# Kernel tuning notes

Measured on AMD Instinct MI355X. Metric: run time of the kernel, lower is better.

Reference implementation:

```python
import jax, jax.numpy as jnp
import numpy as np

NUM_HEADS = 8  # matches init_kwargs num_heads
LN_EPS = 1e-5  # torch.nn.LayerNorm default


def setup_inputs() -> dict:
    key = jax.random.key(0)
    ks = jax.random.split(key, 12)
    E, B, H, S = 16384, 16, 256, 32
    edge_features = jax.random.normal(ks[0], (E, H), jnp.float32)
    edge_coords = jax.random.normal(ks[1], (E, 3), jnp.float32)
    # sorted, equal-size segments (all graphs non-empty)
    batch = jnp.repeat(jnp.arange(B, dtype=jnp.int32), E // B)
    s_h = 1.0 / np.sqrt(H)
    s_sh = 1.0 / np.sqrt(S * H)
    seed_vectors = jax.random.normal(ks[2], (S, H), jnp.float32)
    # weights stored [in, out] (transposed vs torch nn.Linear)
    Wq = jax.random.normal(ks[3], (H, H), jnp.float32) * s_h
    Wk = jax.random.normal(ks[4], (H, H), jnp.float32) * s_h
    Wv = jax.random.normal(ks[5], (H, H), jnp.float32) * s_h
    Wo = jax.random.normal(ks[6], (H, H), jnp.float32) * s_h
    bo = jnp.zeros((H,), jnp.float32)
    ln_g = jnp.ones((H,), jnp.float32)
    ln_b = jnp.zeros((H,), jnp.float32)
    W1 = jax.random.normal(ks[7], (S * H, H), jnp.float32) * s_sh
    b1 = jnp.zeros((H,), jnp.float32)
    W2 = jax.random.normal(ks[8], (H, H), jnp.float32) * s_h
    b2 = jnp.zeros((H,), jnp.float32)
    return dict(edge_features=edge_features, edge_coords=edge_coords, batch=batch,
                seed_vectors=seed_vectors, Wq=Wq, Wk=Wk, Wv=Wv, Wo=Wo, bo=bo,
                ln_g=ln_g, ln_b=ln_b, W1=W1, b1=b1, W2=W2, b2=b2, num_graphs=B)


def reference(edge_features, edge_coords, batch, seed_vectors, Wq, Wk, Wv, Wo, bo,
              ln_g, ln_b, W1, b1, W2, b2, num_graphs):
    S, H = seed_vectors.shape
    nh = NUM_HEADS
    hd = H // nh
    q = (seed_vectors @ Wq).reshape(S, nh, hd)          # shared across graphs
    k = (edge_features @ Wk).reshape(-1, nh, hd)        # [E, nh, hd]
    v = (edge_features @ Wv).reshape(-1, nh, hd)
    scores = jnp.einsum('shd,ehd->esh', q, k) / np.sqrt(hd).astype(np.float32)
    # segment softmax over edges within each graph
    m = jax.lax.stop_gradient(jax.ops.segment_max(scores, batch, num_segments=num_graphs))
    num = jnp.exp(scores - m[batch])
    den = jax.ops.segment_sum(num, batch, num_segments=num_graphs)
    w = num / den[batch]                                # [E, S, nh]
    att = jax.ops.segment_sum(jnp.einsum('esh,ehd->eshd', w, v), batch,
                              num_segments=num_graphs)  # [B, S, nh, hd]
    att = att.reshape(num_graphs, S, H)                 # concat heads (head-major)
    y = seed_vectors[None, :, :] + att @ Wo + bo        # residual + out_proj
    mu = jnp.mean(y, axis=-1, keepdims=True)
    var = jnp.mean((y - mu) ** 2, axis=-1, keepdims=True)
    y = (y - mu) / jnp.sqrt(var + LN_EPS) * ln_g + ln_b
    flat = y.reshape(num_graphs, S * H)
    h1 = jax.nn.silu(flat @ W1 + b1)
    return h1 @ W2 + b2                                 # [B, H]
```

## Files before the change

### kernel.cpp

```cpp
#include <hip/hip_runtime.h>
#include <math.h>
#include <stdint.h>

#define E_EDGES 16384
#define H_DIM   256
#define S_SEEDS 32
#define NHEADS  8
#define HDIM    32
#define BGRAPHS 16
#define EPG     1024
#define NCHUNK  256
#define CPG     16
#define RSQRT_HD 0.17677669529663687f

typedef __attribute__((ext_vector_type(8))) short bf16x8;
typedef __attribute__((ext_vector_type(4))) float f32x4;

__device__ inline unsigned short f2bf(float x) {
    unsigned u = __float_as_uint(x);
    u += 0x7fff + ((u >> 16) & 1);
    return (unsigned short)(u >> 16);
}
__device__ inline float bf2f(unsigned int h) {
    return __uint_as_float((h & 0xffffu) << 16);
}
__device__ inline unsigned pack2(float a, float b) {
    return (unsigned)f2bf(a) | ((unsigned)f2bf(b) << 16);
}

__global__ __launch_bounds__(256) void k_wc(const float* __restrict__ Wv,
                                            const float* __restrict__ Wk,
                                            const float* __restrict__ Wq,
                                            const float* __restrict__ seed,
                                            unsigned short* __restrict__ WcT) {
    int j = blockIdx.x;
    int i = threadIdx.x;
    float val;
    if (j < H_DIM) {
        val = Wv[i * H_DIM + j];
    } else {
        int c = j - H_DIM;
        int h = c >> 5, s = c & 31;
        __shared__ float qp[8][33];
        __shared__ float qrow[HDIM];
        int d = i & 31, g = i >> 5;
        const float* wq = &Wq[(g * 32) * H_DIM + h * HDIM + d];
        const float* sd = &seed[s * H_DIM + g * 32];
        float p = 0.f;
        #pragma unroll
        for (int ii = 0; ii < 32; ++ii)
            p = fmaf(sd[ii], wq[(size_t)ii * H_DIM], p);
        qp[g][d] = p;
        __syncthreads();
        if (i < HDIM) {
            float qv = 0.f;
            #pragma unroll
            for (int g2 = 0; g2 < 8; ++g2) qv += qp[g2][i];
            qrow[i] = qv;
        }
        __syncthreads();
        const float* wk = &Wk[i * H_DIM + h * HDIM];
        float acc = 0.f;
        #pragma unroll
        for (int dd = 0; dd < HDIM; dd += 4) {
            float4 w = *(const float4*)&wk[dd];
            float4 qq = *(const float4*)&qrow[dd];
            acc = fmaf(w.x, qq.x, acc); acc = fmaf(w.y, qq.y, acc);
            acc = fmaf(w.z, qq.z, acc); acc = fmaf(w.w, qq.w, acc);
        }
        val = acc * RSQRT_HD;
    }
    WcT[j * H_DIM + i] = f2bf(val);
}

struct SMattn {
    unsigned short As[64][264];
    unsigned short Vt[256][72];
    unsigned short Pt[256][72];
};

__global__ __launch_bounds__(512) void k_attn(const float* __restrict__ A,
                                              const unsigned short* __restrict__ WcT,
                                              float* __restrict__ outc,
                                              float* __restrict__ mg,
                                              float* __restrict__ sg) {
    __shared__ SMattn sm;
    int tid = threadIdx.x;
    int chunk = blockIdx.x;
    int e0 = chunk * 64;
    int w = tid >> 6, lane = tid & 63;
    int lr = lane & 15, kg = lane >> 4;

    {
        int r = tid >> 3, cg8 = tid & 7;
        const float* ap = &A[(size_t)(e0 + r) * H_DIM + cg8 * 32];
        #pragma unroll
        for (int i = 0; i < 4; ++i) {
            float4 x = *(const float4*)&ap[i * 8];
            float4 y = *(const float4*)&ap[i * 8 + 4];
            uint4 o;
            o.x = pack2(x.x, x.y); o.y = pack2(x.z, x.w);
            o.z = pack2(y.x, y.y); o.w = pack2(y.z, y.w);
            *(uint4*)&sm.As[r][cg8 * 32 + i * 8] = o;
        }
    }
    __syncthreads();

    const unsigned short* brow = &WcT[(size_t)(w * 64 + lr) * H_DIM + kg * 8];
    uint4 bfr[2][4];
    #pragma unroll
    for (int ni = 0; ni < 4; ++ni) {
        bfr[0][ni] = *(const uint4*)(brow + (size_t)ni * 16 * H_DIM);
        bfr[1][ni] = *(const uint4*)(brow + (size_t)ni * 16 * H_DIM + 32);
    }
    f32x4 acc[4][4] = {};
    #pragma unroll
    for (int k = 0; k < 8; ++k) {
        bf16x8 af[4], bv[4];
        #pragma unroll
        for (int mi = 0; mi < 4; ++mi)
            af[mi] = *(const bf16x8*)&sm.As[mi * 16 + lr][k * 32 + kg * 8];
        #pragma unroll
        for (int ni = 0; ni < 4; ++ni)
            bv[ni] = *(const bf16x8*)&bfr[k & 1][ni];
        if (k < 6) {
            #pragma unroll
            for (int ni = 0; ni < 4; ++ni)
                bfr[k & 1][ni] = *(const uint4*)(brow + (size_t)ni * 16 * H_DIM + (k + 2) * 32);
        }
        #pragma unroll
        for (int mi = 0; mi < 4; ++mi)
            #pragma unroll
            for (int ni = 0; ni < 4; ++ni)
                acc[mi][ni] = __builtin_amdgcn_mfma_f32_16x16x32_bf16(
                    af[mi], bv[ni], acc[mi][ni], 0, 0, 0);
    }

    if (w < 4) {
        #pragma unroll
        for (int mi = 0; mi < 4; ++mi)
            #pragma unroll
            for (int ni = 0; ni < 4; ++ni)
                #pragma unroll
                for (int r = 0; r < 4; ++r)
                    sm.Vt[w * 64 + ni * 16 + lr][mi * 16 + kg * 4 + r] =
                        f2bf(acc[mi][ni][r]);
    } else {
        int wn = (w - 4) * 64;
        #pragma unroll
        for (int ni = 0; ni < 4; ++ni) {
            float m = -1e30f;
            #pragma unroll
            for (int mi = 0; mi < 4; ++mi)
                #pragma unroll
                for (int r = 0; r < 4; ++r) m = fmaxf(m, acc[mi][ni][r]);
            m = fmaxf(m, __shfl_xor(m, 16, 64));
            m = fmaxf(m, __shfl_xor(m, 32, 64));
            float sv = 0.f;
            #pragma unroll
            for (int mi = 0; mi < 4; ++mi)
                #pragma unroll
                for (int r = 0; r < 4; ++r) {
                    float e_ = __expf(acc[mi][ni][r] - m);
                    unsigned short eb = f2bf(e_);
                    sm.Pt[wn + ni * 16 + lr][mi * 16 + kg * 4 + r] = eb;
                    sv += bf2f(eb);
                }
            sv += __shfl_xor(sv, 16, 64);
            sv += __shfl_xor(sv, 32, 64);
            if (kg == 0) {
                mg[(size_t)chunk * H_DIM + wn + ni * 16 + lr] = m;
                sg[(size_t)chunk * H_DIM + wn + ni * 16 + lr] = sv;
            }
        }
    }
    __syncthreads();

    f32x4 acc2[2][2] = {};
    #pragma unroll
    for (int ms = 0; ms < 2; ++ms)
        #pragma unroll
        for (int nd = 0; nd < 2; ++nd)
            #pragma unroll
            for (int kk = 0; kk < 2; ++kk) {
                bf16x8 pa = *(const bf16x8*)&sm.Pt[w * 32 + ms * 16 + lr][kk * 32 + kg * 8];
                bf16x8 vb = *(const bf16x8*)&sm.Vt[w * 32 + nd * 16 + lr][kk * 32 + kg * 8];
                acc2[ms][nd] = __builtin_amdgcn_mfma_f32_16x16x32_bf16(
                    pa, vb, acc2[ms][nd], 0, 0, 0);
            }
    #pragma unroll
    for (int ms = 0; ms < 2; ++ms)
        #pragma unroll
        for (int nd = 0; nd < 2; ++nd)
            #pragma unroll
            for (int r = 0; r < 4; ++r) {
                int s_ = ms * 16 + kg * 4 + r;
                int c_ = w * 32 + nd * 16 + lr;
                outc[((size_t)chunk * 32 + s_) * H_DIM + c_] = acc2[ms][nd][r];
            }
}

__device__ inline float block_sum256(float v, float* red4) {
    for (int o = 32; o > 0; o >>= 1) v += __shfl_xor(v, o, 64);
    int wid = threadIdx.x >> 6;
    if ((threadIdx.x & 63) == 0) red4[wid] = v;
    __syncthreads();
    float r = red4[0] + red4[1] + red4[2] + red4[3];
    __syncthreads();
    return r;
}

__global__ __launch_bounds__(256) void k_tail(const float* __restrict__ outc,
                                              const float* __restrict__ mg,
                                              const float* __restrict__ sg,
                                              const float* __restrict__ seed,
                                              const float* __restrict__ Wo,
                                              const float* __restrict__ bo,
                                              const float* __restrict__ ln_g,
                                              const float* __restrict__ ln_b,
                                              const float* __restrict__ W1,
                                              float* __restrict__ part) {
    int bs = blockIdx.x;
    int b = bs >> 5, s = bs & 31;
    int c = threadIdx.x;
    __shared__ float mjv[CPG][8], sgv[CPG][8], sscale[CPG][8];
    __shared__ float arow[H_DIM];
    __shared__ float ynorm[H_DIM];
    __shared__ float red4[4];
    if (c < 128) {
        int j = c >> 3, h = c & 7;
        int sc = h * 32 + s;
        mjv[j][h] = mg[(size_t)(b * CPG + j) * H_DIM + sc];
        sgv[j][h] = sg[(size_t)(b * CPG + j) * H_DIM + sc];
    }
    __syncthreads();
    if (c < 8) {
        int h = c;
        float M = -1e30f;
        #pragma unroll
        for (int j = 0; j < CPG; ++j) M = fmaxf(M, mjv[j][h]);
        float Den = 0.f;
        #pragma unroll
        for (int j = 0; j < CPG; ++j) Den += sgv[j][h] * __expf(mjv[j][h] - M);
        float inv = 1.f / Den;
        #pragma unroll
        for (int j = 0; j < CPG; ++j) sscale[j][h] = __expf(mjv[j][h] - M) * inv;
    }
    __syncthreads();
    {
        int h = c >> 5;
        float a = 0.f;
        #pragma unroll
        for (int j = 0; j < CPG; ++j)
            a = fmaf(outc[((size_t)(b * CPG + j) * 32 + s) * H_DIM + c],
                     sscale[j][h], a);
        arow[c] = a;
    }
    __syncthreads();
    float y = bo[c] + seed[s * H_DIM + c];
    #pragma unroll 1
    for (int i = 0; i < H_DIM; i += 32) {
        float wv[32];
        #pragma unroll
        for (int k = 0; k < 32; ++k)
            wv[k] = Wo[(size_t)(i + k) * H_DIM + c];
        #pragma unroll
        for (int k = 0; k < 32; ++k)
            y = fmaf(arow[i + k], wv[k], y);
    }
    float mu = block_sum256(y, red4) * (1.f / 256.f);
    float d = y - mu;
    float var = block_sum256(d * d, red4) * (1.f / 256.f);
    ynorm[c] = d * rsqrtf(var + 1e-5f) * ln_g[c] + ln_b[c];
    __syncthreads();
    {
        const float* w1p = &W1[(size_t)(s * H_DIM) * H_DIM + c];
        float acc = 0.f;
        #pragma unroll 1
        for (int i = 0; i < H_DIM; i += 32) {
            float wv[32];
            #pragma unroll
            for (int k = 0; k < 32; ++k)
                wv[k] = w1p[(size_t)(i + k) * H_DIM];
            #pragma unroll
            for (int k = 0; k < 32; ++k)
                acc = fmaf(ynorm[i + k], wv[k], acc);
        }
        part[((size_t)s * BGRAPHS + b) * H_DIM + c] = acc;
    }
}

__global__ __launch_bounds__(1024) void k_mlp2(const float* __restrict__ part,
                                               const float* __restrict__ b1,
                                               const float* __restrict__ W2,
                                               const float* __restrict__ b2,
                                               float* __restrict__ out) {
    int b = blockIdx.x;
    int t = threadIdx.x;
    int c = t & 255, g = t >> 8;
    __shared__ float red[4][H_DIM];
    __shared__ float hrow[H_DIM];
    float sacc = 0.f;
    #pragma unroll
    for (int sc2 = g * 8; sc2 < g * 8 + 8; ++sc2)
        sacc += part[((size_t)sc2 * BGRAPHS + b) * H_DIM + c];
    red[g][c] = sacc;
    __syncthreads();
    if (g == 0) {
        float s = red[0][c] + red[1][c] + red[2][c] + red[3][c] + b1[c];
        hrow[c] = s / (1.f + __expf(-s));
    }
    __syncthreads();
    float wacc = 0.f;
    #pragma unroll 4
    for (int j = g * 64; j < g * 64 + 64; ++j)
        wacc = fmaf(hrow[j], W2[(size_t)j * H_DIM + c], wacc);
    red[g][c] = wacc;
    __syncthreads();
    if (g == 0)
        out[(size_t)b * H_DIM + c] = red[0][c] + red[1][c] + red[2][c] + red[3][c] + b2[c];
}

extern "C" void kernel_launch(void* const* d_in, const int* in_sizes, int n_in,
                              void* d_out, int out_size, void* d_ws, size_t ws_size,
                              hipStream_t stream) {
    const float* edge_features = (const float*)d_in[0];
    const float* seed = (const float*)d_in[3];
    const float* Wq   = (const float*)d_in[4];
    const float* Wk   = (const float*)d_in[5];
    const float* Wv   = (const float*)d_in[6];
    const float* Wo   = (const float*)d_in[7];
    const float* bo   = (const float*)d_in[8];
    const float* ln_g = (const float*)d_in[9];
    const float* ln_b = (const float*)d_in[10];
    const float* W1   = (const float*)d_in[11];
    const float* b1   = (const float*)d_in[12];
    const float* W2   = (const float*)d_in[13];
    const float* b2   = (const float*)d_in[14];
    float* out = (float*)d_out;

    float* ws = (float*)d_ws;
    unsigned short* WcT = (unsigned short*)ws;
    float* outc = ws + 65536;
    float* mg   = outc + 2097152;
    float* sg   = mg + 65536;
    float* part = sg + 65536;

    k_wc   <<<512, 256, 0, stream>>>(Wv, Wk, Wq, seed, WcT);
    k_attn <<<NCHUNK, 512, 0, stream>>>(edge_features, WcT, outc, mg, sg);
    k_tail <<<512, 256, 0, stream>>>(outc, mg, sg, seed, Wo, bo, ln_g, ln_b, W1, part);
    k_mlp2 <<<BGRAPHS, 1024, 0, stream>>>(part, b1, W2, b2, out);
}
```

Baseline: 134.4 us.

## Fuse attention, tail and MLP kernels into one persistent kernel with grid barriers

```diff
diff --git a/kernel.cpp b/kernel.cpp
--- a/kernel.cpp
+++ b/kernel.cpp
@@ -32,9 +32,11 @@
                                             const float* __restrict__ Wk,
                                             const float* __restrict__ Wq,
                                             const float* __restrict__ seed,
-                                            unsigned short* __restrict__ WcT) {
+                                            unsigned short* __restrict__ WcT,
+                                            unsigned int* __restrict__ counters) {
     int j = blockIdx.x;
     int i = threadIdx.x;
+    if (j == 0 && i < 2) counters[i] = 0u;
     float val;
     if (j < H_DIM) {
         val = Wv[i * H_DIM + j];
@@ -78,247 +80,271 @@
     unsigned short Vt[256][72];
     unsigned short Pt[256][72];
 };
-
-__global__ __launch_bounds__(512) void k_attn(const float* __restrict__ A,
-                                              const unsigned short* __restrict__ WcT,
-                                              float* __restrict__ outc,
-                                              float* __restrict__ mg,
-                                              float* __restrict__ sg) {
-    __shared__ SMattn sm;
+struct SMtail {
+    float mjv[2][CPG][8], sgv[2][CPG][8], sscale[2][CPG][8];
+    float arow[2][H_DIM];
+    float ynorm[2][H_DIM];
+    float red[2][4];
+};
+struct SMm2 { float red[2][H_DIM]; float hrow[H_DIM]; };
+
+__device__ inline void grid_sync(unsigned int* cnt) {
+    __threadfence();
+    __syncthreads();
+    if (threadIdx.x == 0) {
+        __hip_atomic_fetch_add(cnt, 1u, __ATOMIC_ACQ_REL, __HIP_MEMORY_SCOPE_AGENT);
+        while (__hip_atomic_load(cnt, __ATOMIC_ACQUIRE, __HIP_MEMORY_SCOPE_AGENT) < 256u) {}
+    }
+    __syncthreads();
+    __threadfence();
+}
+
+__global__ __launch_bounds__(512) void k_fused(
+        const float* __restrict__ A,    const unsigned short* __restrict__ WcT,
+        const float* __restrict__ seed, const float* __restrict__ Wo,
+        const float* __restrict__ bo,   const float* __restrict__ ln_g,
+        const float* __restrict__ ln_b, const float* __restrict__ W1,
+        const float* __restrict__ b1,   const float* __restrict__ W2,
+        const float* __restrict__ b2,   float* __restrict__ outc,
+        float* __restrict__ mg,         float* __restrict__ sg,
+        float* __restrict__ part,       unsigned int* __restrict__ counters,
+        float* __restrict__ out) {
+    __shared__ union { SMattn attn; SMtail tail; SMm2 m2; } smu;
     int tid = threadIdx.x;
-    int chunk = blockIdx.x;
-    int e0 = chunk * 64;
-    int w = tid >> 6, lane = tid & 63;
-    int lr = lane & 15, kg = lane >> 4;
 
     {
-        int r = tid >> 3, cg8 = tid & 7;
-        const float* ap = &A[(size_t)(e0 + r) * H_DIM + cg8 * 32];
-        #pragma unroll
-        for (int i = 0; i < 4; ++i) {
-            float4 x = *(const float4*)&ap[i * 8];
-            float4 y = *(const float4*)&ap[i * 8 + 4];
-            uint4 o;
-            o.x = pack2(x.x, x.y); o.y = pack2(x.z, x.w);
-            o.z = pack2(y.x, y.y); o.w = pack2(y.z, y.w);
-            *(uint4*)&sm.As[r][cg8 * 32 + i * 8] = o;
-        }
-    }
-    __syncthreads();
-
-    const unsigned short* brow = &WcT[(size_t)(w * 64 + lr) * H_DIM + kg * 8];
-    uint4 bfr[2][4];
-    #pragma unroll
-    for (int ni = 0; ni < 4; ++ni) {
-        bfr[0][ni] = *(const uint4*)(brow + (size_t)ni * 16 * H_DIM);
-        bfr[1][ni] = *(const uint4*)(brow + (size_t)ni * 16 * H_DIM + 32);
-    }
-    f32x4 acc[4][4] = {};
-    #pragma unroll
-    for (int k = 0; k < 8; ++k) {
-        bf16x8 af[4], bv[4];
-        #pragma unroll
-        for (int mi = 0; mi < 4; ++mi)
-            af[mi] = *(const bf16x8*)&sm.As[mi * 16 + lr][k * 32 + kg * 8];
-        #pragma unroll
-        for (int ni = 0; ni < 4; ++ni)
-            bv[ni] = *(const bf16x8*)&bfr[k & 1][ni];
-        if (k < 6) {
+        SMattn& sm = smu.attn;
+        int chunk = blockIdx.x;
+        int e0 = chunk * 64;
+        int w = tid >> 6, lane = tid & 63;
+        int lr = lane & 15, kg = lane >> 4;
+
+        {
+            int r = tid >> 3, cg8 = tid & 7;
+            const float* ap = &A[(size_t)(e0 + r) * H_DIM + cg8 * 32];
+            #pragma unroll
+            for (int i = 0; i < 4; ++i) {
+                float4 x = *(const float4*)&ap[i * 8];
+                float4 y = *(const float4*)&ap[i * 8 + 4];
+                uint4 o;
+                o.x = pack2(x.x, x.y); o.y = pack2(x.z, x.w);
+                o.z = pack2(y.x, y.y); o.w = pack2(y.z, y.w);
+                *(uint4*)&sm.As[r][cg8 * 32 + i * 8] = o;
+            }
+        }
+        __syncthreads();
+
+        const unsigned short* brow = &WcT[(size_t)(w * 64 + lr) * H_DIM + kg * 8];
+        uint4 bfr[2][4];
+        #pragma unroll
+        for (int ni = 0; ni < 4; ++ni) {
+            bfr[0][ni] = *(const uint4*)(brow + (size_t)ni * 16 * H_DIM);
+            bfr[1][ni] = *(const uint4*)(brow + (size_t)ni * 16 * H_DIM + 32);
+        }
+        f32x4 acc[4][4] = {};
+        #pragma unroll
+        for (int k = 0; k < 8; ++k) {
+            bf16x8 af[4], bv[4];
+            #pragma unroll
+            for (int mi = 0; mi < 4; ++mi)
+                af[mi] = *(const bf16x8*)&sm.As[mi * 16 + lr][k * 32 + kg * 8];
             #pragma unroll
             for (int ni = 0; ni < 4; ++ni)
-                bfr[k & 1][ni] = *(const uint4*)(brow + (size_t)ni * 16 * H_DIM + (k + 2) * 32);
-        }
-        #pragma unroll
-        for (int mi = 0; mi < 4; ++mi)
-            #pragma unroll
-            for (int ni = 0; ni < 4; ++ni)
-                acc[mi][ni] = __builtin_amdgcn_mfma_f32_16x16x32_bf16(
-                    af[mi], bv[ni], acc[mi][ni], 0, 0, 0);
-    }
-
-    if (w < 4) {
-        #pragma unroll
-        for (int mi = 0; mi < 4; ++mi)
-            #pragma unroll
-            for (int ni = 0; ni < 4; ++ni)
-                #pragma unroll
-                for (int r = 0; r < 4; ++r)
-                    sm.Vt[w * 64 + ni * 16 + lr][mi * 16 + kg * 4 + r] =
-                        f2bf(acc[mi][ni][r]);
-    } else {
-        int wn = (w - 4) * 64;
-        #pragma unroll
-        for (int ni = 0; ni < 4; ++ni) {
-            float m = -1e30f;
+                bv[ni] = *(const bf16x8*)&bfr[k & 1][ni];
+            if (k < 6) {
+                #pragma unroll
+                for (int ni = 0; ni < 4; ++ni)
+                    bfr[k & 1][ni] = *(const uint4*)(brow + (size_t)ni * 16 * H_DIM + (k + 2) * 32);
+            }
             #pragma unroll
             for (int mi = 0; mi < 4; ++mi)
                 #pragma unroll
-                for (int r = 0; r < 4; ++r) m = fmaxf(m, acc[mi][ni][r]);
-            m = fmaxf(m, __shfl_xor(m, 16, 64));
-            m = fmaxf(m, __shfl_xor(m, 32, 64));
-            float sv = 0.f;
+                for (int ni = 0; ni < 4; ++ni)
+                    acc[mi][ni] = __builtin_amdgcn_mfma_f32_16x16x32_bf16(
+                        af[mi], bv[ni], acc[mi][ni], 0, 0, 0);
+        }
+
+        if (w < 4) {
             #pragma unroll
             for (int mi = 0; mi < 4; ++mi)
                 #pragma unroll
+                for (int ni = 0; ni < 4; ++ni)
+                    #pragma unroll
+                    for (int r = 0; r < 4; ++r)
+                        sm.Vt[w * 64 + ni * 16 + lr][mi * 16 + kg * 4 + r] =
+                            f2bf(acc[mi][ni][r]);
+        } else {
+            int wn = (w - 4) * 64;
+            #pragma unroll
+            for (int ni = 0; ni < 4; ++ni) {
+                float m = -1e30f;
+                #pragma unroll
+                for (int mi = 0; mi < 4; ++mi)
+                    #pragma unroll
+                    for (int r = 0; r < 4; ++r) m = fmaxf(m, acc[mi][ni][r]);
+                m = fmaxf(m, __shfl_xor(m, 16, 64));
+                m = fmaxf(m, __shfl_xor(m, 32, 64));
+                float sv = 0.f;
+                #pragma unroll
+                for (int mi = 0; mi < 4; ++mi)
+                    #pragma unroll
+                    for (int r = 0; r < 4; ++r) {
+                        float e_ = __expf(acc[mi][ni][r] - m);
+                        unsigned short eb = f2bf(e_);
+                        sm.Pt[wn + ni * 16 + lr][mi * 16 + kg * 4 + r] = eb;
+                        sv += bf2f(eb);
+                    }
+                sv += __shfl_xor(sv, 16, 64);
+                sv += __shfl_xor(sv, 32, 64);
+                if (kg == 0) {
+                    mg[(size_t)chunk * H_DIM + wn + ni * 16 + lr] = m;
+                    sg[(size_t)chunk * H_DIM + wn + ni * 16 + lr] = sv;
+                }
+            }
+        }
+        __syncthreads();
+
+        f32x4 acc2[2][2] = {};
+        #pragma unroll
+        for (int ms = 0; ms < 2; ++ms)
+            #pragma unroll
+            for (int nd = 0; nd < 2; ++nd)
+                #pragma unroll
+                for (int kk = 0; kk < 2; ++kk) {
+                    bf16x8 pa = *(const bf16x8*)&sm.Pt[w * 32 + ms * 16 + lr][kk * 32 + kg * 8];
+                    bf16x8 vb = *(const bf16x8*)&sm.Vt[w * 32 + nd * 16 + lr][kk * 32 + kg * 8];
+                    acc2[ms][nd] = __builtin_amdgcn_mfma_f32_16x16x32_bf16(
+                        pa, vb, acc2[ms][nd], 0, 0, 0);
+                }
+        #pragma unroll
+        for (int ms = 0; ms < 2; ++ms)
+            #pragma unroll
+            for (int nd = 0; nd < 2; ++nd)
+                #pragma unroll
                 for (int r = 0; r < 4; ++r) {
-                    float e_ = __expf(acc[mi][ni][r] - m);
-                    unsigned short eb = f2bf(e_);
-                    sm.Pt[wn + ni * 16 + lr][mi * 16 + kg * 4 + r] = eb;
-                    sv += bf2f(eb);
+                    int s_ = ms * 16 + kg * 4 + r;
+                    int c_ = w * 32 + nd * 16 + lr;
+                    outc[((size_t)chunk * 32 + s_) * H_DIM + c_] = acc2[ms][nd][r];
                 }
-            sv += __shfl_xor(sv, 16, 64);
-            sv += __shfl_xor(sv, 32, 64);
-            if (kg == 0) {
-                mg[(size_t)chunk * H_DIM + wn + ni * 16 + lr] = m;
-                sg[(size_t)chunk * H_DIM + wn + ni * 16 + lr] = sv;
-            }
-        }
-    }
-    __syncthreads();
-
-    f32x4 acc2[2][2] = {};
-    #pragma unroll
-    for (int ms = 0; ms < 2; ++ms)
-        #pragma unroll
-        for (int nd = 0; nd < 2; ++nd)
-            #pragma unroll
-            for (int kk = 0; kk < 2; ++kk) {
-                bf16x8 pa = *(const bf16x8*)&sm.Pt[w * 32 + ms * 16 + lr][kk * 32 + kg * 8];
-                bf16x8 vb = *(const bf16x8*)&sm.Vt[w * 32 + nd * 16 + lr][kk * 32 + kg * 8];
-                acc2[ms][nd] = __builtin_amdgcn_mfma_f32_16x16x32_bf16(
-                    pa, vb, acc2[ms][nd], 0, 0, 0);
-            }
-    #pragma unroll
-    for (int ms = 0; ms < 2; ++ms)
-        #pragma unroll
-        for (int nd = 0; nd < 2; ++nd)
-            #pragma unroll
-            for (int r = 0; r < 4; ++r) {
-                int s_ = ms * 16 + kg * 4 + r;
-                int c_ = w * 32 + nd * 16 + lr;
-                outc[((size_t)chunk * 32 + s_) * H_DIM + c_] = acc2[ms][nd][r];
-            }
-}
-
-__device__ inline float block_sum256(float v, float* red4) {
-    for (int o = 32; o > 0; o >>= 1) v += __shfl_xor(v, o, 64);
-    int wid = threadIdx.x >> 6;
-    if ((threadIdx.x & 63) == 0) red4[wid] = v;
-    __syncthreads();
-    float r = red4[0] + red4[1] + red4[2] + red4[3];
-    __syncthreads();
-    return r;
-}
-
-__global__ __launch_bounds__(256) void k_tail(const float* __restrict__ outc,
-                                              const float* __restrict__ mg,
-                                              const float* __restrict__ sg,
-                                              const float* __restrict__ seed,
-                                              const float* __restrict__ Wo,
-                                              const float* __restrict__ bo,
-                                              const float* __restrict__ ln_g,
-                                              const float* __restrict__ ln_b,
-                                              const float* __restrict__ W1,
-                                              float* __restrict__ part) {
-    int bs = blockIdx.x;
-    int b = bs >> 5, s = bs & 31;
-    int c = threadIdx.x;
-    __shared__ float mjv[CPG][8], sgv[CPG][8], sscale[CPG][8];
-    __shared__ float arow[H_DIM];
-    __shared__ float ynorm[H_DIM];
-    __shared__ float red4[4];
-    if (c < 128) {
-        int j = c >> 3, h = c & 7;
-        int sc = h * 32 + s;
-        mjv[j][h] = mg[(size_t)(b * CPG + j) * H_DIM + sc];
-        sgv[j][h] = sg[(size_t)(b * CPG + j) * H_DIM + sc];
-    }
-    __syncthreads();
-    if (c < 8) {
-        int h = c;
-        float M = -1e30f;
-        #pragma unroll
-        for (int j = 0; j < CPG; ++j) M = fmaxf(M, mjv[j][h]);
-        float Den = 0.f;
-        #pragma unroll
-        for (int j = 0; j < CPG; ++j) Den += sgv[j][h] * __expf(mjv[j][h] - M);
-        float inv = 1.f / Den;
-        #pragma unroll
-        for (int j = 0; j < CPG; ++j) sscale[j][h] = __expf(mjv[j][h] - M) * inv;
-    }
-    __syncthreads();
+    }
+    grid_sync(&counters[0]);
+
     {
-        int h = c >> 5;
-        float a = 0.f;
-        #pragma unroll
-        for (int j = 0; j < CPG; ++j)
-            a = fmaf(outc[((size_t)(b * CPG + j) * 32 + s) * H_DIM + c],
-                     sscale[j][h], a);
-        arow[c] = a;
-    }
-    __syncthreads();
-    float y = bo[c] + seed[s * H_DIM + c];
-    #pragma unroll 1
-    for (int i = 0; i < H_DIM; i += 32) {
-        float wv[32];
-        #pragma unroll
-        for (int k = 0; k < 32; ++k)
-            wv[k] = Wo[(size_t)(i + k) * H_DIM + c];
-        #pragma unroll
-        for (int k = 0; k < 32; ++k)
-            y = fmaf(arow[i + k], wv[k], y);
-    }
-    float mu = block_sum256(y, red4) * (1.f / 256.f);
-    float d = y - mu;
-    float var = block_sum256(d * d, red4) * (1.f / 256.f);
-    ynorm[c] = d * rsqrtf(var + 1e-5f) * ln_g[c] + ln_b[c];
-    __syncthreads();
-    {
-        const float* w1p = &W1[(size_t)(s * H_DIM) * H_DIM + c];
-        float acc = 0.f;
+        SMtail& t = smu.tail;
+        int half = tid >> 8, tl = tid & 255;
+        int bs = blockIdx.x * 2 + half;
+        int b = bs >> 5, s = bs & 31;
+        if (tl < 128) {
+            int j = tl >> 3, h = tl & 7;
+            int sc = h * 32 + s;
+            t.mjv[half][j][h] = mg[(size_t)(b * CPG + j) * H_DIM + sc];
+            t.sgv[half][j][h] = sg[(size_t)(b * CPG + j) * H_DIM + sc];
+        }
+        __syncthreads();
+        if (tl < 8) {
+            int h = tl;
+            float M = -1e30f;
+            #pragma unroll
+            for (int j = 0; j < CPG; ++j) M = fmaxf(M, t.mjv[half][j][h]);
+            float Den = 0.f;
+            #pragma unroll
+            for (int j = 0; j < CPG; ++j)
+                Den += t.sgv[half][j][h] * __expf(t.mjv[half][j][h] - M);
+            float inv = 1.f / Den;
+            #pragma unroll
+            for (int j = 0; j < CPG; ++j)
+                t.sscale[half][j][h] = __expf(t.mjv[half][j][h] - M) * inv;
+        }
+        __syncthreads();
+        {
+            int h = tl >> 5;
+            float a = 0.f;
+            #pragma unroll
+            for (int j = 0; j < CPG; ++j)
+                a = fmaf(outc[((size_t)(b * CPG + j) * 32 + s) * H_DIM + tl],
+                         t.sscale[half][j][h], a);
+            t.arow[half][tl] = a;
+        }
+        __syncthreads();
+        float y = bo[tl] + seed[s * H_DIM + tl];
         #pragma unroll 1
         for (int i = 0; i < H_DIM; i += 32) {
             float wv[32];
             #pragma unroll
             for (int k = 0; k < 32; ++k)
-                wv[k] = w1p[(size_t)(i + k) * H_DIM];
+                wv[k] = Wo[(size_t)(i + k) * H_DIM + tl];
             #pragma unroll
             for (int k = 0; k < 32; ++k)
-                acc = fmaf(ynorm[i + k], wv[k], acc);
-        }
-        part[((size_t)s * BGRAPHS + b) * H_DIM + c] = acc;
-    }
-}
-
-__global__ __launch_bounds__(1024) void k_mlp2(const float* __restrict__ part,
-                                               const float* __restrict__ b1,
-                                               const float* __restrict__ W2,
-                                               const float* __restrict__ b2,
-                                               float* __restrict__ out) {
-    int b = blockIdx.x;
-    int t = threadIdx.x;
-    int c = t & 255, g = t >> 8;
-    __shared__ float red[4][H_DIM];
-    __shared__ float hrow[H_DIM];
-    float sacc = 0.f;
-    #pragma unroll
-    for (int sc2 = g * 8; sc2 < g * 8 + 8; ++sc2)
-        sacc += part[((size_t)sc2 * BGRAPHS + b) * H_DIM + c];
-    red[g][c] = sacc;
-    __syncthreads();
-    if (g == 0) {
-        float s = red[0][c] + red[1][c] + red[2][c] + red[3][c] + b1[c];
-        hrow[c] = s / (1.f + __expf(-s));
-    }
-    __syncthreads();
-    float wacc = 0.f;
-    #pragma unroll 4
-    for (int j = g * 64; j < g * 64 + 64; ++j)
-        wacc = fmaf(hrow[j], W2[(size_t)j * H_DIM + c], wacc);
-    red[g][c] = wacc;
-    __syncthreads();
-    if (g == 0)
-        out[(size_t)b * H_DIM + c] = red[0][c] + red[1][c] + red[2][c] + red[3][c] + b2[c];
+                y = fmaf(t.arow[half][i + k], wv[k], y);
+        }
+        int wid4 = (tid >> 6) & 3;
+        float v = y;
+        #pragma unroll
+        for (int o = 32; o > 0; o >>= 1) v += __shfl_xor(v, o, 64);
+        if ((tid & 63) == 0) t.red[half][wid4] = v;
+        __syncthreads();
+        float mu = (t.red[half][0] + t.red[half][1] + t.red[half][2] + t.red[half][3])
+                   * (1.f / 256.f);
+        __syncthreads();
+        float d = y - mu;
+        v = d * d;
+        #pragma unroll
+        for (int o = 32; o > 0; o >>= 1) v += __shfl_xor(v, o, 64);
+        if ((tid & 63) == 0) t.red[half][wid4] = v;
+        __syncthreads();
+        float var = (t.red[half][0] + t.red[half][1] + t.red[half][2] + t.red[half][3])
+                    * (1.f / 256.f);
+        t.ynorm[half][tl] = d * rsqrtf(var + 1e-5f) * ln_g[tl] + ln_b[tl];
+        __syncthreads();
+        {
+            const float* w1p = &W1[(size_t)(s * H_DIM) * H_DIM + tl];
+            float acc = 0.f;
+            #pragma unroll 1
+            for (int i = 0; i < H_DIM; i += 32) {
+                float wv[32];
+                #pragma unroll
+                for (int k = 0; k < 32; ++k)
+                    wv[k] = w1p[(size_t)(i + k) * H_DIM];
+                #pragma unroll
+                for (int k = 0; k < 32; ++k)
+                    acc = fmaf(t.ynorm[half][i + k], wv[k], acc);
+            }
+            part[((size_t)s * BGRAPHS + b) * H_DIM + tl] = acc;
+        }
+    }
+    grid_sync(&counters[1]);
+
+    if (blockIdx.x < 16) {
+        SMm2& m = smu.m2;
+        int b = blockIdx.x;
+        int c = tid & 255, g = tid >> 8;
+        float sacc = 0.f;
+        #pragma unroll
+        for (int sc2 = g * 16; sc2 < g * 16 + 16; ++sc2)
+            sacc += part[((size_t)sc2 * BGRAPHS + b) * H_DIM + c];
+        m.red[g][c] = sacc;
+        __syncthreads();
+        if (g == 0) {
+            float s = m.red[0][c] + m.red[1][c] + b1[c];
+            m.hrow[c] = s / (1.f + __expf(-s));
+        }
+        __syncthreads();
+        float wacc = 0.f;
+        #pragma unroll 1
+        for (int j0 = g * 128; j0 < g * 128 + 128; j0 += 32) {
+            float wv[32];
+            #pragma unroll
+            for (int k = 0; k < 32; ++k)
+                wv[k] = W2[(size_t)(j0 + k) * H_DIM + c];
+            #pragma unroll
+            for (int k = 0; k < 32; ++k)
+                wacc = fmaf(m.hrow[j0 + k], wv[k], wacc);
+        }
+        m.red[g][c] = wacc;
+        __syncthreads();
+        if (g == 0)
+            out[(size_t)b * H_DIM + c] = m.red[0][c] + m.red[1][c] + b2[c];
+    }
 }
 
 extern "C" void kernel_launch(void* const* d_in, const int* in_sizes, int n_in,
@@ -345,9 +371,10 @@
     float* mg   = outc + 2097152;
     float* sg   = mg + 65536;
     float* part = sg + 65536;
-
-    k_wc   <<<512, 256, 0, stream>>>(Wv, Wk, Wq, seed, WcT);
-    k_attn <<<NCHUNK, 512, 0, stream>>>(edge_features, WcT, outc, mg, sg);
-    k_tail <<<512, 256, 0, stream>>>(outc, mg, sg, seed, Wo, bo, ln_g, ln_b, W1, part);
-    k_mlp2 <<<BGRAPHS, 1024, 0, stream>>>(part, b1, W2, b2, out);
-}
+    unsigned int* counters = (unsigned int*)(part + 131072);
+
+    k_wc    <<<512, 256, 0, stream>>>(Wv, Wk, Wq, seed, WcT, counters);
+    k_fused <<<NCHUNK, 512, 0, stream>>>(edge_features, WcT, seed, Wo, bo, ln_g,
+                                         ln_b, W1, b1, W2, b2, outc, mg, sg,
+                                         part, counters, out);
+}
```

Measured after the change: 305.9 us. 128% more time.
